# Performance work log

Measured on AMD Instinct MI355X. Metric: run time of the kernel, lower is better.

## Reference

```python
import jax, jax.numpy as jnp
import numpy as np

WIN = (7, 7)
NUM_HEADS = 12
LORA_SCALING = 16.0 / 16.0  # lora_alpha / lora_rank


def _relative_position_index(win):
    wh, ww = win
    coords = np.stack(np.meshgrid(np.arange(wh), np.arange(ww), indexing='ij'))  # (2, wh, ww)
    cf = coords.reshape(2, -1)
    rel = cf[:, :, None] - cf[:, None, :]  # (2, N, N)
    rel = rel.transpose(1, 2, 0)
    rel[:, :, 0] += wh - 1
    rel[:, :, 1] += ww - 1
    rel[:, :, 0] *= 2 * ww - 1
    return jnp.asarray(rel.sum(-1), dtype=jnp.int32)  # (N, N)


def setup_inputs() -> dict:
    key = jax.random.key(0)
    ks = jax.random.split(key, 12)
    B_, N, C, r = 2048, 49, 384, 16
    nW = 64
    s = 0.02
    return {
        'x': jax.random.normal(ks[0], (B_, N, C), jnp.float32),
        'mask': jnp.zeros((nW, N, N), jnp.float32),
        'qkv_w': jax.random.normal(ks[1], (C, 3 * C), jnp.float32) * s,
        'qkv_b': jax.random.normal(ks[2], (3 * C,), jnp.float32) * s,
        'qa_w': jax.random.normal(ks[3], (C, r), jnp.float32) * s,
        'qb_w': jax.random.normal(ks[4], (r, C), jnp.float32) * s,
        'va_w': jax.random.normal(ks[5], (C, r), jnp.float32) * s,
        'vb_w': jax.random.normal(ks[6], (r, C), jnp.float32) * s,
        'rpb_table': jax.random.normal(ks[7], ((2 * WIN[0] - 1) * (2 * WIN[1] - 1), NUM_HEADS), jnp.float32) * s,
        'proj_w': jax.random.normal(ks[8], (C, C), jnp.float32) * s,
        'proj_b': jax.random.normal(ks[9], (C,), jnp.float32) * s,
    }


def reference(x, mask, qkv_w, qkv_b, qa_w, qb_w, va_w, vb_w, rpb_table, proj_w, proj_b):
    B_, N, C = x.shape
    H = NUM_HEADS
    hd = C // H
    scale = hd ** -0.5

    qkv = (x @ qkv_w + qkv_b).reshape(B_, N, 3, H, hd)
    qkv = jnp.transpose(qkv, (2, 0, 3, 1, 4))  # (3, B_, H, N, hd)
    q, k, v = qkv[0], qkv[1], qkv[2]

    q_lora = LORA_SCALING * ((x @ qa_w) @ qb_w)  # (B_, N, C)
    q = q + jnp.transpose(q_lora.reshape(B_, N, H, hd), (0, 2, 1, 3))
    v_lora = LORA_SCALING * ((x @ va_w) @ vb_w)
    v = v + jnp.transpose(v_lora.reshape(B_, N, H, hd), (0, 2, 1, 3))

    attn = jnp.einsum('bhnd,bhmd->bhnm', q * scale, k)  # (B_, H, N, N)

    rel_idx = _relative_position_index(WIN)  # (N, N) static int
    rpb = rpb_table[rel_idx]  # (N, N, H)
    attn = attn + jnp.transpose(rpb, (2, 0, 1))[None]

    nW = mask.shape[0]
    attn = attn.reshape(B_ // nW, nW, H, N, N) + mask[None, :, None]
    attn = attn.reshape(B_, H, N, N)
    attn = jax.nn.softmax(attn, axis=-1)

    out = jnp.einsum('bhnm,bhmd->bhnd', attn, v)
    out = jnp.transpose(out, (0, 2, 1, 3)).reshape(B_, N, C)
    return out @ proj_w + proj_b
```

## Files before the change

kernel.cpp:

```cpp
#include <hip/hip_runtime.h>
#include <hip/hip_bf16.h>

typedef __hip_bfloat16 bf16;
typedef float f32x4 __attribute__((ext_vector_type(4)));
typedef short bf16x8 __attribute__((ext_vector_type(8)));

static __device__ __forceinline__ void gload_lds16(const void* g, void* l) {
    __builtin_amdgcn_global_load_lds(
        (const __attribute__((address_space(1))) void*)g,
        (__attribute__((address_space(3))) void*)l, 16, 0, 0);
}

static __device__ __forceinline__ short bf16bits(float v) {
    bf16 tb = __float2bfloat16(v);
    return *reinterpret_cast<short*>(&tb);
}

static __device__ __forceinline__ float exp2_fast(float x) {
    float r;
    asm("v_exp_f32 %0, %1" : "=v"(r) : "v"(x));
    return r;
}

__global__ __launch_bounds__(256) void cvt_x_kernel(const float4* __restrict__ x,
                                                    bf16* __restrict__ xb, int n4) {
    int i = blockIdx.x * 256 + threadIdx.x;
    const int stride = gridDim.x * 256;
    for (; i < n4; i += stride) {
        float4 v = x[i];
        alignas(8) bf16 tmp[4];
        tmp[0] = __float2bfloat16(v.x);
        tmp[1] = __float2bfloat16(v.y);
        tmp[2] = __float2bfloat16(v.z);
        tmp[3] = __float2bfloat16(v.w);
        *reinterpret_cast<uint2*>(xb + 4l * i) = *reinterpret_cast<uint2*>(tmp);
    }
}

__global__ __launch_bounds__(256) void build_wefft_kernel(
    const float* __restrict__ qkv_w, const float* __restrict__ qa,
    const float* __restrict__ qb, const float* __restrict__ va,
    const float* __restrict__ vb, bf16* __restrict__ wt) {
    int idx = blockIdx.x * 256 + threadIdx.x;
    int ncol = idx / 384;
    int k = idx - ncol * 384;
    float v = qkv_w[k * 1152 + ncol];
    if (ncol < 384) {
        float s = 0.f;
#pragma unroll
        for (int j = 0; j < 16; ++j) s += qa[k * 16 + j] * qb[j * 384 + ncol];
        v += s;
    } else if (ncol >= 768) {
        int nc = ncol - 768;
        float s = 0.f;
#pragma unroll
        for (int j = 0; j < 16; ++j) s += va[k * 16 + j] * vb[j * 384 + nc];
        v += s;
    }
    wt[(long)ncol * 384 + k] = __float2bfloat16(v);
}

__global__ __launch_bounds__(256) void build_projt_kernel(const float* __restrict__ pw,
                                                          bf16* __restrict__ pt) {
    int idx = blockIdx.x * 256 + threadIdx.x;
    int ncol = idx / 384;
    int k = idx - ncol * 384;
    pt[(long)ncol * 384 + k] = __float2bfloat16(pw[k * 384 + ncol]);
}

__global__ __launch_bounds__(256) void build_cbias_kernel(const float* __restrict__ rpb_table,
                                                          const float* __restrict__ mask,
                                                          float* __restrict__ cbias) {
    int idx = blockIdx.x * 256 + threadIdx.x;
    int h = idx >> 18;
    int w = (idx >> 12) & 63;
    int ij = idx & 4095;
    int i = ij >> 6, j = ij & 63;
    float v;
    if (j < 49) {
        if (i < 49) {
            int yi = i / 7, xi = i - yi * 7;
            int yj = j / 7, xj = j - yj * 7;
            int rel = (yi - yj + 6) * 13 + (xi - xj + 6);
            v = (rpb_table[rel * 12 + h] + mask[w * 2401 + i * 49 + j]) * 1.4426950408889634f;
        } else {
            v = 0.f;
        }
    } else {
        v = -1e30f;
    }
    cbias[idx] = v;
}

template <bool OUT_BF16>
__global__ __launch_bounds__(256) void gemm_kernel(const bf16* __restrict__ A,
                                                   const bf16* __restrict__ BT,
                                                   const float* __restrict__ bias,
                                                   void* __restrict__ Cout,
                                                   int N, int K, int nxb, int nwg) {
    __shared__ short Al[128 * 64];
    __shared__ short Bl[128 * 64];
    const int t = threadIdx.x;
    const int lane = t & 63;
    const int wave = t >> 6;
    const int wr = wave >> 1;
    const int wc = wave & 1;
    const int g = lane >> 4, c = lane & 15;

    const int q8 = nwg >> 3;
    const int wgid = (blockIdx.x & 7) * q8 + (blockIdx.x >> 3);
    const int by = wgid / nxb;
    const int bx = wgid - by * nxb;
    const long rowBase = (long)by * 128;
    const long colBase = (long)bx * 128;

    f32x4 acc[4][4];
#pragma unroll
    for (int m = 0; m < 4; ++m)
#pragma unroll
        for (int n = 0; n < 4; ++n) acc[m][n] = (f32x4){0.f, 0.f, 0.f, 0.f};

    for (int k0 = 0; k0 < K; k0 += 64) {
        __syncthreads();
#pragma unroll
        for (int it = 0; it < 4; ++it) {
            int chunk = it * 256 + t;
            int row = chunk >> 3;
            int blk = lane & 7;
            gload_lds16(A + (size_t)(rowBase + row) * K + k0 + ((blk ^ (row & 7)) * 8),
                        &Al[(it * 256 + wave * 64) * 8]);
            gload_lds16(BT + (size_t)(colBase + row) * K + k0 + ((blk ^ (row & 7)) * 8),
                        &Bl[(it * 256 + wave * 64) * 8]);
        }
        asm volatile("s_waitcnt vmcnt(0)" ::: "memory");
        __syncthreads();

#pragma unroll
        for (int ks = 0; ks < 2; ++ks) {
            bf16x8 af[4], bfr[4];
#pragma unroll
            for (int m = 0; m < 4; ++m) {
                int row = wr * 64 + m * 16 + c;
                af[m] = *(const bf16x8*)&Al[row * 64 + (((ks * 4 + g) ^ (c & 7)) * 8)];
            }
#pragma unroll
            for (int n = 0; n < 4; ++n) {
                int row = wc * 64 + n * 16 + c;
                bfr[n] = *(const bf16x8*)&Bl[row * 64 + (((ks * 4 + g) ^ (c & 7)) * 8)];
            }
#pragma unroll
            for (int m = 0; m < 4; ++m)
#pragma unroll
                for (int n = 0; n < 4; ++n)
                    acc[m][n] = __builtin_amdgcn_mfma_f32_16x16x32_bf16(af[m], bfr[n],
                                                                        acc[m][n], 0, 0, 0);
        }
    }

    const int crow0 = wr * 64 + g * 4;
    const long ccol0 = colBase + wc * 64 + c;
#pragma unroll
    for (int m = 0; m < 4; ++m) {
#pragma unroll
        for (int n = 0; n < 4; ++n) {
            const long col = ccol0 + n * 16;
            const float bv = bias[col];
#pragma unroll
            for (int r = 0; r < 4; ++r) {
                const long row = rowBase + crow0 + m * 16 + r;
                float v = acc[m][n][r] + bv;
                if (OUT_BF16)
                    ((bf16*)Cout)[row * N + col] = __float2bfloat16(v);
                else
                    ((float*)Cout)[row * N + col] = v;
            }
        }
    }
}

__global__ __launch_bounds__(256) void attn_kernel(const bf16* __restrict__ qkv,
                                                   const float* __restrict__ cbias,
                                                   bf16* __restrict__ out) {
    __shared__ short lds[4 * 6144];
    const int t = threadIdx.x, lane = t & 63, wave = t >> 6;
    short* W = lds + wave * 6144;
    const int bh = blockIdx.x * 4 + wave;
    const int b = bh / 12, h = bh - b * 12;
    const int g = lane >> 4, c = lane & 15;
    const int w = b & 63;
    const size_t base = (size_t)b * 49 * 1152 + h * 32;
    const float scale2 = 0.17677669529663687f * 1.4426950408889634f;

    uint4 vr[3], vt4;
#pragma unroll
    for (int it = 0; it < 3; ++it) {
        int c4 = it * 64 + lane;
        int n = c4 >> 2, o = (c4 & 3) * 8;
        vr[it] = *(const uint4*)(qkv + base + (size_t)n * 1152 + 768 + o);
    }
    vt4 = *(const uint4*)(qkv + base + (size_t)48 * 1152 + 768 + (lane & 3) * 8);

    bf16x8 aq[4], bk[4];
#pragma unroll
    for (int mt = 0; mt < 4; ++mt) {
        int row = mt * 16 + c;
        row = row > 48 ? 48 : row;
        aq[mt] = *(const bf16x8*)(qkv + base + (size_t)row * 1152 + g * 8);
        bk[mt] = *(const bf16x8*)(qkv + base + (size_t)row * 1152 + 384 + g * 8);
    }

#pragma unroll
    for (int z = 0; z < 4; ++z)
        *(uint4*)&W[4096 + (z * 64 + lane) * 8] = (uint4){0u, 0u, 0u, 0u};

    const float* cb = cbias + ((size_t)((h << 6) | w) << 12);
    float inv[16];
#pragma unroll
    for (int mt = 0; mt < 4; ++mt) {
        f32x4 Sv[4];
#pragma unroll
        for (int nt = 0; nt < 4; ++nt)
            Sv[nt] = __builtin_amdgcn_mfma_f32_16x16x32_bf16(aq[mt], bk[nt],
                                                             (f32x4){0.f, 0.f, 0.f, 0.f}, 0, 0, 0);
        const int rowoff = (mt * 16 + g * 4) << 6;
#pragma unroll
        for (int nt = 0; nt < 4; ++nt) {
            int j = nt * 16 + c;
#pragma unroll
            for (int r = 0; r < 4; ++r)
                Sv[nt][r] = fmaf(Sv[nt][r], scale2, cb[rowoff + (r << 6) + j]);
        }
#pragma unroll
        for (int r = 0; r < 4; ++r) {
            float s = 0.f;
#pragma unroll
            for (int nt = 0; nt < 4; ++nt) {
                float e = exp2_fast(Sv[nt][r]);
                Sv[nt][r] = e;
                s += e;
            }
            s += __shfl_xor(s, 1);
            s += __shfl_xor(s, 2);
            s += __shfl_xor(s, 4);
            s += __shfl_xor(s, 8);
            inv[mt * 4 + r] = 1.f / s;
        }
#pragma unroll
        for (int r = 0; r < 4; ++r) {
            const int i = mt * 16 + g * 4 + r;
            const int ix = (i & 7) << 3;
#pragma unroll
            for (int nt = 0; nt < 4; ++nt) {
                unsigned my = (unsigned)(unsigned short)bf16bits(Sv[nt][r]);
                unsigned oth = (unsigned)__builtin_amdgcn_mov_dpp((int)my, 0xB1, 0xF, 0xF, true);
                unsigned pair = (c & 1) ? (oth | (my << 16)) : (my | (oth << 16));
                const bool doit = (c & 1) ? (nt >= 2) : (nt < 2);
                if (doit) {
                    int j0 = nt * 16 + (c & ~1);
                    *(unsigned*)&W[i * 64 + (j0 ^ ix)] = pair;
                }
            }
        }
    }

#pragma unroll
    for (int it = 0; it < 3; ++it) {
        int c4 = it * 64 + lane;
        int n = c4 >> 2, o = (c4 & 3) * 8;
        alignas(16) short tmp[8];
        *(uint4*)tmp = vr[it];
#pragma unroll
        for (int j = 0; j < 8; ++j) {
            int d = o + j;
            W[4096 + ((d * 64 + n) ^ ((d & 7) << 3))] = tmp[j];
        }
    }
    if (lane < 4) {
        int o = (lane & 3) * 8;
        alignas(16) short tmp[8];
        *(uint4*)tmp = vt4;
#pragma unroll
        for (int j = 0; j < 8; ++j) {
            int d = o + j;
            W[4096 + ((d * 64 + 48) ^ ((d & 7) << 3))] = tmp[j];
        }
    }

    f32x4 O[4][2];
#pragma unroll
    for (int mt = 0; mt < 4; ++mt)
#pragma unroll
        for (int dt = 0; dt < 2; ++dt) O[mt][dt] = (f32x4){0.f, 0.f, 0.f, 0.f};
#pragma unroll
    for (int ks = 0; ks < 2; ++ks) {
        bf16x8 pa[4], vb2[2];
#pragma unroll
        for (int mt = 0; mt < 4; ++mt) {
            int i = mt * 16 + c;
            pa[mt] = *(const bf16x8*)&W[(i * 64 + ks * 32 + g * 8) ^ ((i & 7) << 3)];
        }
#pragma unroll
        for (int dt = 0; dt < 2; ++dt) {
            int d = dt * 16 + c;
            vb2[dt] = *(const bf16x8*)&W[4096 + ((d * 64 + ks * 32 + g * 8) ^ ((d & 7) << 3))];
        }
#pragma unroll
        for (int mt = 0; mt < 4; ++mt)
#pragma unroll
            for (int dt = 0; dt < 2; ++dt)
                O[mt][dt] = __builtin_amdgcn_mfma_f32_16x16x32_bf16(pa[mt], vb2[dt],
                                                                    O[mt][dt], 0, 0, 0);
    }

#pragma unroll
    for (int mt = 0; mt < 4; ++mt)
#pragma unroll
        for (int r = 0; r < 4; ++r) {
            int i = mt * 16 + g * 4 + r;
            const float iv = inv[mt * 4 + r];
            unsigned pair[2];
#pragma unroll
            for (int dt = 0; dt < 2; ++dt) {
                unsigned my = (unsigned)(unsigned short)bf16bits(O[mt][dt][r] * iv);
                unsigned oth = (unsigned)__builtin_amdgcn_mov_dpp((int)my, 0xB1, 0xF, 0xF, true);
                pair[dt] = my | (oth << 16);
            }
            if (i < 49 && !(c & 1)) {
                bf16* dst = out + ((size_t)(b * 49 + i)) * 384 + h * 32 + c;
                *(unsigned*)(dst) = pair[0];
                *(unsigned*)(dst + 16) = pair[1];
            }
        }
}

extern "C" void kernel_launch(void* const* d_in, const int* in_sizes, int n_in,
                              void* d_out, int out_size, void* d_ws, size_t ws_size,
                              hipStream_t stream) {
    (void)in_sizes; (void)n_in; (void)out_size; (void)ws_size;
    const float* x      = (const float*)d_in[0];
    const float* mask   = (const float*)d_in[1];
    const float* qkv_w  = (const float*)d_in[2];
    const float* qkv_b  = (const float*)d_in[3];
    const float* qa_w   = (const float*)d_in[4];
    const float* qb_w   = (const float*)d_in[5];
    const float* va_w   = (const float*)d_in[6];
    const float* vb_w   = (const float*)d_in[7];
    const float* rpb    = (const float*)d_in[8];
    const float* proj_w = (const float*)d_in[9];
    const float* proj_b = (const float*)d_in[10];

    char* ws = (char*)d_ws;
    bf16* xb     = (bf16*)(ws);
    bf16* attno  = (bf16*)(ws);
    bf16* wefft  = (bf16*)(ws + 77070336);
    bf16* projt  = (bf16*)(ws + 77955072);
    float* cbias = (float*)(ws + 78249984);
    bf16* qkv    = (bf16*)(ws + 90832896);

    cvt_x_kernel<<<2048, 256, 0, stream>>>((const float4*)x, xb, 9633792);
    build_wefft_kernel<<<1728, 256, 0, stream>>>(qkv_w, qa_w, qb_w, va_w, vb_w, wefft);
    build_projt_kernel<<<576, 256, 0, stream>>>(proj_w, projt);
    build_cbias_kernel<<<12288, 256, 0, stream>>>(rpb, mask, cbias);
    gemm_kernel<true><<<3528, 256, 0, stream>>>(xb, wefft, qkv_b, qkv, 1152, 384, 9, 3528);
    gemm_kernel<true><<<3528, 256, 0, stream>>>(xb + (size_t)50176 * 384, wefft, qkv_b,
                                                qkv + (size_t)50176 * 1152, 1152, 384, 9, 3528);
    attn_kernel<<<6144, 256, 0, stream>>>(qkv, cbias, attno);
    gemm_kernel<false><<<2352, 256, 0, stream>>>(attno, projt, proj_b, d_out, 384, 384, 3, 2352);
}
```

Before: 364.4 us.

## Use ds_read_b64_tr_b16 for V transpose and transpose combined bias layout

V tiles are now stored to LDS with 16-byte vector writes in their natural layout, and the hardware transposing LDS read (ds_read_b64_tr_b16) builds the MFMA B operand. This replaces the per-element scalar transposed LDS stores. The combined bias buffer is laid out transposed so each lane fetches its four row values with one float4 load instead of four strided scalar loads. A manual lgkmcnt wait and sched_barrier are added, which may limit the compiler's ability to overlap LDS reads with MFMA work.

```diff
diff --git a/kernel.cpp b/kernel.cpp
--- a/kernel.cpp
+++ b/kernel.cpp
@@ -4,6 +4,7 @@
 typedef __hip_bfloat16 bf16;
 typedef float f32x4 __attribute__((ext_vector_type(4)));
 typedef short bf16x8 __attribute__((ext_vector_type(8)));
+typedef short short4v __attribute__((ext_vector_type(4)));
 
 static __device__ __forceinline__ void gload_lds16(const void* g, void* l) {
     __builtin_amdgcn_global_load_lds(
@@ -19,6 +20,15 @@
 static __device__ __forceinline__ float exp2_fast(float x) {
     float r;
     asm("v_exp_f32 %0, %1" : "=v"(r) : "v"(x));
+    return r;
+}
+
+static __device__ __forceinline__ short4v tr_b64(const short* p) {
+    short4v r;
+    asm volatile("ds_read_b64_tr_b16 %0, %1"
+                 : "=v"(r)
+                 : "v"((const __attribute__((address_space(3))) short*)p)
+                 : "memory");
     return r;
 }
 
@@ -74,8 +84,8 @@
     int idx = blockIdx.x * 256 + threadIdx.x;
     int h = idx >> 18;
     int w = (idx >> 12) & 63;
-    int ij = idx & 4095;
-    int i = ij >> 6, j = ij & 63;
+    int j = (idx >> 6) & 63;
+    int i = idx & 63;
     float v;
     if (j < 49) {
         if (i < 49) {
@@ -209,11 +219,9 @@
         bk[mt] = *(const bf16x8*)(qkv + base + (size_t)row * 1152 + 384 + g * 8);
     }
 
-#pragma unroll
-    for (int z = 0; z < 4; ++z)
-        *(uint4*)&W[4096 + (z * 64 + lane) * 8] = (uint4){0u, 0u, 0u, 0u};
-
-    const float* cb = cbias + ((size_t)((h << 6) | w) << 12);
+    *(uint4*)&W[4096 + 1536 + lane * 8] = (uint4){0u, 0u, 0u, 0u};
+
+    const float* cbT = cbias + ((size_t)((h << 6) | w) << 12);
     float inv[16];
 #pragma unroll
     for (int mt = 0; mt < 4; ++mt) {
@@ -222,13 +230,13 @@
         for (int nt = 0; nt < 4; ++nt)
             Sv[nt] = __builtin_amdgcn_mfma_f32_16x16x32_bf16(aq[mt], bk[nt],
                                                              (f32x4){0.f, 0.f, 0.f, 0.f}, 0, 0, 0);
-        const int rowoff = (mt * 16 + g * 4) << 6;
+        const int i0 = mt * 16 + g * 4;
 #pragma unroll
         for (int nt = 0; nt < 4; ++nt) {
-            int j = nt * 16 + c;
+            f32x4 cbv = *(const f32x4*)(cbT + (((nt * 16 + c) << 6) + i0));
 #pragma unroll
             for (int r = 0; r < 4; ++r)
-                Sv[nt][r] = fmaf(Sv[nt][r], scale2, cb[rowoff + (r << 6) + j]);
+                Sv[nt][r] = fmaf(Sv[nt][r], scale2, cbv[r]);
         }
 #pragma unroll
         for (int r = 0; r < 4; ++r) {
@@ -267,23 +275,13 @@
     for (int it = 0; it < 3; ++it) {
         int c4 = it * 64 + lane;
         int n = c4 >> 2, o = (c4 & 3) * 8;
-        alignas(16) short tmp[8];
-        *(uint4*)tmp = vr[it];
-#pragma unroll
-        for (int j = 0; j < 8; ++j) {
-            int d = o + j;
-            W[4096 + ((d * 64 + n) ^ ((d & 7) << 3))] = tmp[j];
-        }
+        int sub = (n >> 2) * 2 + (o >> 4);
+        *(uint4*)&W[4096 + sub * 64 + (n & 3) * 16 + (o & 15)] = vr[it];
     }
     if (lane < 4) {
-        int o = (lane & 3) * 8;
-        alignas(16) short tmp[8];
-        *(uint4*)tmp = vt4;
-#pragma unroll
-        for (int j = 0; j < 8; ++j) {
-            int d = o + j;
-            W[4096 + ((d * 64 + 48) ^ ((d & 7) << 3))] = tmp[j];
-        }
+        int o = lane * 8;
+        int sub = 24 + (o >> 4);
+        *(uint4*)&W[4096 + sub * 64 + (o & 15)] = vt4;
     }
 
     f32x4 O[4][2];
@@ -293,22 +291,29 @@
         for (int dt = 0; dt < 2; ++dt) O[mt][dt] = (f32x4){0.f, 0.f, 0.f, 0.f};
 #pragma unroll
     for (int ks = 0; ks < 2; ++ks) {
-        bf16x8 pa[4], vb2[2];
+        bf16x8 pa[4], vbf[2];
+#pragma unroll
+        for (int dt = 0; dt < 2; ++dt) {
+            const short* vbase = &W[4096 + (ks * 16 + g * 4 + dt) * 64 + c * 4];
+            short4v lo = tr_b64(vbase);
+            short4v hi = tr_b64(vbase + 128);
+            bf16x8 v8;
+            v8[0] = lo[0]; v8[1] = lo[1]; v8[2] = lo[2]; v8[3] = lo[3];
+            v8[4] = hi[0]; v8[5] = hi[1]; v8[6] = hi[2]; v8[7] = hi[3];
+            vbf[dt] = v8;
+        }
 #pragma unroll
         for (int mt = 0; mt < 4; ++mt) {
             int i = mt * 16 + c;
             pa[mt] = *(const bf16x8*)&W[(i * 64 + ks * 32 + g * 8) ^ ((i & 7) << 3)];
         }
-#pragma unroll
-        for (int dt = 0; dt < 2; ++dt) {
-            int d = dt * 16 + c;
-            vb2[dt] = *(const bf16x8*)&W[4096 + ((d * 64 + ks * 32 + g * 8) ^ ((d & 7) << 3))];
-        }
+        asm volatile("s_waitcnt lgkmcnt(0)" ::: "memory");
+        __builtin_amdgcn_sched_barrier(0);
 #pragma unroll
         for (int mt = 0; mt < 4; ++mt)
 #pragma unroll
             for (int dt = 0; dt < 2; ++dt)
-                O[mt][dt] = __builtin_amdgcn_mfma_f32_16x16x32_bf16(pa[mt], vb2[dt],
+                O[mt][dt] = __builtin_amdgcn_mfma_f32_16x16x32_bf16(pa[mt], vbf[dt],
                                                                     O[mt][dt], 0, 0, 0);
     }
 
```

After: 381.5 us. +4.7%, slower.

## Use 256x128-tile double-buffered 8-wave GEMM for QKV and transpose bias layout

Applied to the files above, without the earlier changes.

Replaces the two QKV GEMM launches with one 512-thread kernel that computes 256x128 output tiles, double-buffers A/B tiles in LDS through direct global-to-LDS loads, and interleaves prefetch with MFMA phases using barriers and setprio. The combined bias table is stored transposed, so the attention kernel reads four consecutive bias values as one vector load instead of four scalar loads. The larger tile and doubled LDS footprint may reduce occupancy, and the QKV output stores remain scalar bf16 writes.

```diff
diff --git a/kernel.cpp b/kernel.cpp
--- a/kernel.cpp
+++ b/kernel.cpp
@@ -74,8 +74,8 @@
     int idx = blockIdx.x * 256 + threadIdx.x;
     int h = idx >> 18;
     int w = (idx >> 12) & 63;
-    int ij = idx & 4095;
-    int i = ij >> 6, j = ij & 63;
+    int j = (idx >> 6) & 63;
+    int i = idx & 63;
     float v;
     if (j < 49) {
         if (i < 49) {
@@ -90,6 +90,109 @@
         v = -1e30f;
     }
     cbias[idx] = v;
+}
+
+__global__ __launch_bounds__(512) void gemm8p_kernel(const bf16* __restrict__ A,
+                                                     const bf16* __restrict__ BT,
+                                                     const float* __restrict__ bias,
+                                                     bf16* __restrict__ Cout, int nwg) {
+    __shared__ short Al[2][256 * 64];
+    __shared__ short Bl[2][128 * 64];
+    const int t = threadIdx.x, lane = t & 63, wave = t >> 6;
+    const int wr = wave >> 1;
+    const int wc = wave & 1;
+    const int g = lane >> 4, c = lane & 15;
+
+    const int q8 = nwg >> 3;
+    const int wgid = (blockIdx.x & 7) * q8 + (blockIdx.x >> 3);
+    const int by = wgid / 9;
+    const int bx = wgid - by * 9;
+    const long rowBase = (long)by * 256;
+    const long colBase = (long)bx * 128;
+
+    f32x4 acc[4][4];
+#pragma unroll
+    for (int m = 0; m < 4; ++m)
+#pragma unroll
+        for (int n = 0; n < 4; ++n) acc[m][n] = (f32x4){0.f, 0.f, 0.f, 0.f};
+
+    auto stageA = [&](int buf, int k0, int it) {
+        int chunk = it * 512 + t;
+        int row = chunk >> 3;
+        int blk = lane & 7;
+        gload_lds16(A + (size_t)(rowBase + row) * 384 + k0 + ((blk ^ (row & 7)) * 8),
+                    &Al[buf][(it * 512 + wave * 64) * 8]);
+    };
+    auto stageB = [&](int buf, int k0, int it) {
+        int chunk = it * 512 + t;
+        int row = chunk >> 3;
+        int blk = lane & 7;
+        gload_lds16(BT + (size_t)(colBase + row) * 384 + k0 + ((blk ^ (row & 7)) * 8),
+                    &Bl[buf][(it * 512 + wave * 64) * 8]);
+    };
+
+    stageA(0, 0, 0); stageA(0, 0, 1); stageA(0, 0, 2); stageA(0, 0, 3);
+    stageB(0, 0, 0); stageB(0, 0, 1);
+    __syncthreads();
+
+    int cur = 0;
+    for (int kt = 0; kt < 6; ++kt) {
+        const int k0n = (kt + 1) << 6;
+        const bool pf = (kt < 5);
+#pragma unroll
+        for (int p = 0; p < 4; ++p) {
+            if (pf) {
+                if (p == 0) { stageA(cur ^ 1, k0n, 0); stageB(cur ^ 1, k0n, 0); stageA(cur ^ 1, k0n, 1); }
+                else if (p == 1) { stageB(cur ^ 1, k0n, 1); stageA(cur ^ 1, k0n, 2); stageA(cur ^ 1, k0n, 3); }
+            }
+            const int qm = p & 1, qn = p >> 1;
+            bf16x8 af[2][2], bfq[2][2];
+#pragma unroll
+            for (int m2 = 0; m2 < 2; ++m2) {
+                int row = wr * 64 + (qm * 2 + m2) * 16 + c;
+#pragma unroll
+                for (int ks = 0; ks < 2; ++ks)
+                    af[m2][ks] = *(const bf16x8*)&Al[cur][row * 64 + (((ks * 4 + g) ^ (c & 7)) * 8)];
+            }
+#pragma unroll
+            for (int n2 = 0; n2 < 2; ++n2) {
+                int row = wc * 64 + (qn * 2 + n2) * 16 + c;
+#pragma unroll
+                for (int ks = 0; ks < 2; ++ks)
+                    bfq[n2][ks] = *(const bf16x8*)&Bl[cur][row * 64 + (((ks * 4 + g) ^ (c & 7)) * 8)];
+            }
+            __builtin_amdgcn_s_barrier();
+            __builtin_amdgcn_s_setprio(1);
+#pragma unroll
+            for (int ks = 0; ks < 2; ++ks)
+#pragma unroll
+                for (int m2 = 0; m2 < 2; ++m2)
+#pragma unroll
+                    for (int n2 = 0; n2 < 2; ++n2)
+                        acc[qm * 2 + m2][qn * 2 + n2] = __builtin_amdgcn_mfma_f32_16x16x32_bf16(
+                            af[m2][ks], bfq[n2][ks], acc[qm * 2 + m2][qn * 2 + n2], 0, 0, 0);
+            __builtin_amdgcn_s_setprio(0);
+            __builtin_amdgcn_s_barrier();
+        }
+        __syncthreads();
+        cur ^= 1;
+    }
+
+    const int crow0 = wr * 64 + g * 4;
+    const long ccol0 = colBase + wc * 64 + c;
+#pragma unroll
+    for (int m = 0; m < 4; ++m) {
+#pragma unroll
+        for (int n = 0; n < 4; ++n) {
+            const long col = ccol0 + n * 16;
+            const float bv = bias[col];
+#pragma unroll
+            for (int r = 0; r < 4; ++r) {
+                const long row = rowBase + crow0 + m * 16 + r;
+                Cout[row * 1152 + col] = __float2bfloat16(acc[m][n][r] + bv);
+            }
+        }
+    }
 }
 
 template <bool OUT_BF16>
@@ -213,7 +316,7 @@
     for (int z = 0; z < 4; ++z)
         *(uint4*)&W[4096 + (z * 64 + lane) * 8] = (uint4){0u, 0u, 0u, 0u};
 
-    const float* cb = cbias + ((size_t)((h << 6) | w) << 12);
+    const float* cbT = cbias + ((size_t)((h << 6) | w) << 12);
     float inv[16];
 #pragma unroll
     for (int mt = 0; mt < 4; ++mt) {
@@ -222,13 +325,13 @@
         for (int nt = 0; nt < 4; ++nt)
             Sv[nt] = __builtin_amdgcn_mfma_f32_16x16x32_bf16(aq[mt], bk[nt],
                                                              (f32x4){0.f, 0.f, 0.f, 0.f}, 0, 0, 0);
-        const int rowoff = (mt * 16 + g * 4) << 6;
+        const int i0 = mt * 16 + g * 4;
 #pragma unroll
         for (int nt = 0; nt < 4; ++nt) {
-            int j = nt * 16 + c;
+            f32x4 cbv = *(const f32x4*)(cbT + (((nt * 16 + c) << 6) + i0));
 #pragma unroll
             for (int r = 0; r < 4; ++r)
-                Sv[nt][r] = fmaf(Sv[nt][r], scale2, cb[rowoff + (r << 6) + j]);
+                Sv[nt][r] = fmaf(Sv[nt][r], scale2, cbv[r]);
         }
 #pragma unroll
         for (int r = 0; r < 4; ++r) {
@@ -276,7 +379,7 @@
         }
     }
     if (lane < 4) {
-        int o = (lane & 3) * 8;
+        int o = lane * 8;
         alignas(16) short tmp[8];
         *(uint4*)tmp = vt4;
 #pragma unroll
@@ -361,9 +464,7 @@
     build_wefft_kernel<<<1728, 256, 0, stream>>>(qkv_w, qa_w, qb_w, va_w, vb_w, wefft);
     build_projt_kernel<<<576, 256, 0, stream>>>(proj_w, projt);
     build_cbias_kernel<<<12288, 256, 0, stream>>>(rpb, mask, cbias);
-    gemm_kernel<true><<<3528, 256, 0, stream>>>(xb, wefft, qkv_b, qkv, 1152, 384, 9, 3528);
-    gemm_kernel<true><<<3528, 256, 0, stream>>>(xb + (size_t)50176 * 384, wefft, qkv_b,
-                                                qkv + (size_t)50176 * 1152, 1152, 384, 9, 3528);
+    gemm8p_kernel<<<3528, 512, 0, stream>>>(xb, wefft, qkv_b, qkv, 3528);
     attn_kernel<<<6144, 256, 0, stream>>>(qkv, cbias, attno);
     gemm_kernel<false><<<2352, 256, 0, stream>>>(attno, projt, proj_b, d_out, 384, 384, 3, 2352);
 }
```

New measurement: 407.5 us. 1.12x slower.

## Compute softmax row sums via MFMA with ones vector and transpose bias layout

Applied to the files above, without the earlier changes.

The combined bias table is stored transposed so each lane loads four bias values with one vector load instead of four scalar loads. The softmax denominator is no longer reduced with cross-lane shuffles. It is computed by an extra MFMA that multiplies the bf16 probability tile by a ones vector, so the normalisation uses the rounded bf16 probabilities. This removes four shuffle steps per row at the cost of additional MFMA instructions and slightly different rounding.

```diff
diff --git a/kernel.cpp b/kernel.cpp
--- a/kernel.cpp
+++ b/kernel.cpp
@@ -74,8 +74,8 @@
     int idx = blockIdx.x * 256 + threadIdx.x;
     int h = idx >> 18;
     int w = (idx >> 12) & 63;
-    int ij = idx & 4095;
-    int i = ij >> 6, j = ij & 63;
+    int j = (idx >> 6) & 63;
+    int i = idx & 63;
     float v;
     if (j < 49) {
         if (i < 49) {
@@ -213,8 +213,7 @@
     for (int z = 0; z < 4; ++z)
         *(uint4*)&W[4096 + (z * 64 + lane) * 8] = (uint4){0u, 0u, 0u, 0u};
 
-    const float* cb = cbias + ((size_t)((h << 6) | w) << 12);
-    float inv[16];
+    const float* cbT = cbias + ((size_t)((h << 6) | w) << 12);
 #pragma unroll
     for (int mt = 0; mt < 4; ++mt) {
         f32x4 Sv[4];
@@ -222,28 +221,13 @@
         for (int nt = 0; nt < 4; ++nt)
             Sv[nt] = __builtin_amdgcn_mfma_f32_16x16x32_bf16(aq[mt], bk[nt],
                                                              (f32x4){0.f, 0.f, 0.f, 0.f}, 0, 0, 0);
-        const int rowoff = (mt * 16 + g * 4) << 6;
+        const int i0 = mt * 16 + g * 4;
 #pragma unroll
         for (int nt = 0; nt < 4; ++nt) {
-            int j = nt * 16 + c;
+            f32x4 cbv = *(const f32x4*)(cbT + (((nt * 16 + c) << 6) + i0));
 #pragma unroll
             for (int r = 0; r < 4; ++r)
-                Sv[nt][r] = fmaf(Sv[nt][r], scale2, cb[rowoff + (r << 6) + j]);
-        }
-#pragma unroll
-        for (int r = 0; r < 4; ++r) {
-            float s = 0.f;
-#pragma unroll
-            for (int nt = 0; nt < 4; ++nt) {
-                float e = exp2_fast(Sv[nt][r]);
-                Sv[nt][r] = e;
-                s += e;
-            }
-            s += __shfl_xor(s, 1);
-            s += __shfl_xor(s, 2);
-            s += __shfl_xor(s, 4);
-            s += __shfl_xor(s, 8);
-            inv[mt * 4 + r] = 1.f / s;
+                Sv[nt][r] = exp2_fast(fmaf(Sv[nt][r], scale2, cbv[r]));
         }
 #pragma unroll
         for (int r = 0; r < 4; ++r) {
@@ -276,7 +260,7 @@
         }
     }
     if (lane < 4) {
-        int o = (lane & 3) * 8;
+        int o = lane * 8;
         alignas(16) short tmp[8];
         *(uint4*)tmp = vt4;
 #pragma unroll
@@ -286,11 +270,16 @@
         }
     }
 
-    f32x4 O[4][2];
-#pragma unroll
-    for (int mt = 0; mt < 4; ++mt)
+    const short one_bf16 = (short)0x3F80;
+    const bf16x8 vones = {one_bf16, one_bf16, one_bf16, one_bf16,
+                          one_bf16, one_bf16, one_bf16, one_bf16};
+    f32x4 O[4][2], O1[4];
+#pragma unroll
+    for (int mt = 0; mt < 4; ++mt) {
+        O1[mt] = (f32x4){0.f, 0.f, 0.f, 0.f};
 #pragma unroll
         for (int dt = 0; dt < 2; ++dt) O[mt][dt] = (f32x4){0.f, 0.f, 0.f, 0.f};
+    }
 #pragma unroll
     for (int ks = 0; ks < 2; ++ks) {
         bf16x8 pa[4], vb2[2];
@@ -305,11 +294,13 @@
             vb2[dt] = *(const bf16x8*)&W[4096 + ((d * 64 + ks * 32 + g * 8) ^ ((d & 7) << 3))];
         }
 #pragma unroll
-        for (int mt = 0; mt < 4; ++mt)
+        for (int mt = 0; mt < 4; ++mt) {
 #pragma unroll
             for (int dt = 0; dt < 2; ++dt)
                 O[mt][dt] = __builtin_amdgcn_mfma_f32_16x16x32_bf16(pa[mt], vb2[dt],
                                                                     O[mt][dt], 0, 0, 0);
+            O1[mt] = __builtin_amdgcn_mfma_f32_16x16x32_bf16(pa[mt], vones, O1[mt], 0, 0, 0);
+        }
     }
 
 #pragma unroll
@@ -317,7 +308,7 @@
 #pragma unroll
         for (int r = 0; r < 4; ++r) {
             int i = mt * 16 + g * 4 + r;
-            const float iv = inv[mt * 4 + r];
+            const float iv = 1.f / O1[mt][r];
             unsigned pair[2];
 #pragma unroll
             for (int dt = 0; dt < 2; ++dt) {
```

Result: slower. 377.0 us (+3.5%).
